# Optimization experiments

Hardware: AMD Instinct MI355X
Metric: run time of the kernel (lower is better)

Reference implementation:

```python
import jax, jax.numpy as jnp
import numpy as np

N = 65536      # input_size (mesh nodes)
CF = 16        # num_final_channels
L0 = 4097      # inv_conv_start
SPLIT = CF * L0  # 65552
SFC = 2        # number of space-filling curves
LAT = 128      # dims_latent
HID = 512      # size_fc[1]
B = 16         # batch
K = 32         # kernel_size (dimension==2)
STRIDE = 4
PAD = 16       # kernel_size // 2
OUT_PADS = (1, 0)


def setup_inputs() -> dict:
    key = jax.random.key(0)
    ks = jax.random.split(key, 8)
    s = 0.05
    ords, plus, minus = [], [], []
    for i in range(SFC):
        p = np.random.default_rng(i).permutation(N)
        ords.append(p)
        plus.append(np.concatenate([p[1:], p[-1:]]))   # find_plus_neigh
        minus.append(np.concatenate([p[:1], p[:-1]]))  # find_minus_neigh
    return {
        "x": jax.random.normal(ks[0], (B, LAT), jnp.float32),
        "W1": jax.random.normal(ks[1], (HID, LAT), jnp.float32) * s,
        "b1": jnp.zeros((HID,), jnp.float32),
        "W2": jax.random.normal(ks[2], (SPLIT * SFC, HID), jnp.float32) * s,
        "b2": jnp.zeros((SPLIT * SFC,), jnp.float32),
        "ctw0": jax.random.normal(ks[3], (SFC, CF, CF, K), jnp.float32) * s,
        "ctb0": jnp.zeros((SFC, CF), jnp.float32),
        "ctw1": jax.random.normal(ks[4], (SFC, CF, 1, K), jnp.float32) * s,
        "ctb1": jnp.zeros((SFC, 1), jnp.float32),
        "sps_w": jnp.full((SFC, N, 3), 1.0 / 3.0, jnp.float32),   # NearestNeighbouring per-sfc
        "sps_b": jnp.zeros((SFC, N), jnp.float32),
        "final_w": jnp.full((N, SFC), 1.0 / SFC, jnp.float32),    # final_sp
        "final_b": jnp.zeros((N,), jnp.float32),
        "out_w": jnp.ones((N,), jnp.float32),                     # output_linear
        "out_b": jnp.zeros((N,), jnp.float32),
        "ord_idx": jnp.asarray(np.stack(ords), jnp.int32),
        "plus_idx": jnp.asarray(np.stack(plus), jnp.int32),
        "minus_idx": jnp.asarray(np.stack(minus), jnp.int32),
    }


def _convT(b, w, bias, op):
    # PyTorch ConvTranspose1d(w:[Cin,Cout,K], stride=4, padding=16, output_padding=op)
    kern = jnp.flip(w, -1).transpose(1, 0, 2)  # -> [Cout, Cin, K]
    lo = K - 1 - PAD
    out = jax.lax.conv_general_dilated(
        b, kern, window_strides=(1,), padding=[(lo, lo + op)],
        lhs_dilation=(STRIDE,), dimension_numbers=('NCH', 'OIH', 'NCH'))
    return out + bias[None, :, None]


def reference(x, W1, b1, W2, b2, ctw0, ctb0, ctw1, ctb1,
              sps_w, sps_b, final_w, final_b, out_w, out_b,
              ord_idx, plus_idx, minus_idx):
    act = jnp.tanh
    h = act(x @ W1.T + b1)
    h = act(h @ W2.T + b2)
    h = h.reshape(-1, SPLIT, SFC)
    zs = []
    for i in range(SFC):
        b = h[:, :, i].reshape(-1, CF, L0)
        b = act(_convT(b, ctw0[i], ctb0[i], OUT_PADS[0]))  # [B,16,16385]
        b = act(_convT(b, ctw1[i], ctb1[i], OUT_PADS[1]))  # [B,1,65536]
        b = b.reshape(-1, N)
        # SFC gather: (minus, self, plus) neighbours, then learned weighted sum
        tt = jnp.stack([b[:, minus_idx[i]], b[:, ord_idx[i]], b[:, plus_idx[i]]], -1)  # [B,N,3]
        zs.append(act(jnp.sum(tt * sps_w[i], -1) + sps_b[i]))
    z = jnp.stack(zs, -1)                         # [B,N,SFC]
    z = act(jnp.sum(z * final_w, -1) + final_b)   # final NearestNeighbouring across SFCs
    return z * out_w + out_b                      # output_linear (components==1)
```

## Files before the change

kernel.cpp:

```cpp
#include <hip/hip_runtime.h>
#include <hip/hip_bf16.h>

#define N_NODES 65536
#define CFCH 16
#define L0LEN 4097
#define L1LEN 16385
#define NSFC 2
#define LATD 128
#define HIDD 512
#define NROWS (CFCH * L0LEN * NSFC)

typedef __attribute__((ext_vector_type(8))) short short8;
typedef __attribute__((ext_vector_type(4))) float f32x4;

__device__ __forceinline__ float fast_tanh(float x) {
    float ax = fabsf(x);
    float e = __expf(-2.0f * ax);
    float r = (1.0f - e) / (1.0f + e);
    return copysignf(r, x);
}

__device__ __forceinline__ ushort f2bf(float f) {
    unsigned u = __float_as_uint(f);
    return (ushort)((u + 0x7fffu + ((u >> 16) & 1u)) >> 16);
}

__device__ __forceinline__ void split8(const float4 a, const float4 b, short8& hi, short8& lo) {
    float f[8] = {a.x, a.y, a.z, a.w, b.x, b.y, b.z, b.w};
#pragma unroll
    for (int e = 0; e < 8; ++e) {
        ushort h = f2bf(f[e]);
        hi[e] = (short)h;
        lo[e] = (short)f2bf(f[e] - __uint_as_float((unsigned)h << 16));
    }
}

__global__ void fc1_kernel(const float* __restrict__ x, const float* __restrict__ W1,
                           const float* __restrict__ b1,
                           ushort* __restrict__ h1hi, ushort* __restrict__ h1lo) {
    int tid = blockIdx.x * 256 + threadIdx.x;
    int b = tid & 15;
    int j = tid >> 4;
    const float* xr = x + b * LATD;
    const float* wr = W1 + j * LATD;
    float acc = 0.f;
#pragma unroll 8
    for (int k = 0; k < LATD; ++k) acc = fmaf(xr[k], wr[k], acc);
    float h = fast_tanh(acc + b1[j]);
    ushort hi = f2bf(h);
    float hif = __uint_as_float((unsigned)hi << 16);
    ushort lo = f2bf(h - hif);
    h1hi[b * HIDD + j] = hi;
    h1lo[b * HIDD + j] = lo;
}

__global__ void __launch_bounds__(256, 4) fc2_kernel(const float* __restrict__ W2,
                                                     const float* __restrict__ b2,
                                                     const ushort* __restrict__ h1hi,
                                                     const ushort* __restrict__ h1lo,
                                                     float* __restrict__ h2) {
    __shared__ __align__(16) ushort hB[2][16][520];
    for (int u = threadIdx.x; u < 2048; u += 256) {
        int arr = u >> 10, uu = u & 1023;
        int n = uu >> 6, kc = uu & 63;
        const ushort* src = (arr ? h1lo : h1hi) + n * HIDD + kc * 8;
        *(uint4*)&hB[arr][n][kc * 8] = *(const uint4*)src;
    }
    __syncthreads();

    int tid = threadIdx.x;
    int w = tid >> 6, lane = tid & 63;
    int lm = lane & 15, lq = lane >> 4;
    int j0 = blockIdx.x * 128;
    int jr0 = j0 + (w * 2) * 16 + lm;     if (jr0 >= NROWS) jr0 = NROWS - 1;
    int jr1 = j0 + (w * 2 + 1) * 16 + lm; if (jr1 >= NROWS) jr1 = NROWS - 1;
    const float* a0p = W2 + (size_t)jr0 * HIDD + lq * 8;
    const float* a1p = W2 + (size_t)jr1 * HIDD + lq * 8;
    const ushort* bhp = &hB[0][lm][lq * 8];
    const ushort* blp = &hB[1][lm][lq * 8];
    f32x4 acc0 = {0.f, 0.f, 0.f, 0.f};
    f32x4 acc1 = {0.f, 0.f, 0.f, 0.f};

#pragma unroll 2
    for (int ks = 0; ks < 16; ++ks) {
        float4 a0a = *(const float4*)(a0p + ks * 32);
        float4 a0b = *(const float4*)(a0p + ks * 32 + 4);
        float4 a1a = *(const float4*)(a1p + ks * 32);
        float4 a1b = *(const float4*)(a1p + ks * 32 + 4);
        short8 bh = *(const short8*)(bhp + ks * 32);
        short8 bl = *(const short8*)(blp + ks * 32);
        short8 h0, l0, h1v, l1v;
        split8(a0a, a0b, h0, l0);
        split8(a1a, a1b, h1v, l1v);
        acc0 = __builtin_amdgcn_mfma_f32_16x16x32_bf16(h0, bh, acc0, 0, 0, 0);
        acc1 = __builtin_amdgcn_mfma_f32_16x16x32_bf16(h1v, bh, acc1, 0, 0, 0);
        acc0 = __builtin_amdgcn_mfma_f32_16x16x32_bf16(h0, bl, acc0, 0, 0, 0);
        acc1 = __builtin_amdgcn_mfma_f32_16x16x32_bf16(h1v, bl, acc1, 0, 0, 0);
        acc0 = __builtin_amdgcn_mfma_f32_16x16x32_bf16(l0, bh, acc0, 0, 0, 0);
        acc1 = __builtin_amdgcn_mfma_f32_16x16x32_bf16(l1v, bh, acc1, 0, 0, 0);
    }

#pragma unroll
    for (int mt = 0; mt < 2; ++mt) {
        f32x4 acc = mt ? acc1 : acc0;
        int jb = j0 + (w * 2 + mt) * 16 + lq * 4;
#pragma unroll
        for (int reg = 0; reg < 4; ++reg) {
            int j = jb + reg;
            if (j < NROWS) {
                float val = fast_tanh(acc[reg] + b2[j]);
                int ii = j & 1;
                int s = j >> 1;
                int c = s / L0LEN;
                int l = s - c * L0LEN;
                h2[((size_t)(ii * 16 + lm) * CFCH + c) * L0LEN + l] = val;
            }
        }
    }
}

#define SROW 592
#define PHYSF(f) ((f) + (((f) >> 5) << 2))

__global__ void __launch_bounds__(256, 4) conv0_kernel(const float* __restrict__ h2,
                                                       const float* __restrict__ ctw0,
                                                       const float* __restrict__ ctb0,
                                                       float* __restrict__ t0) {
    __shared__ float inS[16 * SROW];
    int bx = blockIdx.x, bb = blockIdx.y, z = blockIdx.z;
    int i = z >> 3;
    int co0 = (z & 7) << 1;
    int tid = threadIdx.x;
    int r = __builtin_amdgcn_readfirstlane(tid >> 6);
    int lane = tid & 63;

    const float* hin = h2 + (size_t)((i * 16 + bb) * 16) * L0LEN;
    int qbase = (bx << 9) - 4;
#pragma unroll 1
    for (int ci = 0; ci < 16; ++ci) {
        for (int xx = tid; xx < 528; xx += 256) {
            int q = qbase + xx;
            inS[ci * SROW + PHYSF(xx)] = (q >= 0 && q < L0LEN) ? hin[ci * L0LEN + q] : 0.f;
        }
    }
    __syncthreads();

    float acc0[8], acc1[8];
#pragma unroll
    for (int u = 0; u < 8; ++u) { acc0[u] = 0.f; acc1[u] = 0.f; }

    const float* wbase = ctw0 + (((i * 16) * 16 + co0) << 5) + r;
    int fb = lane << 3;
#pragma unroll 2
    for (int ci = 0; ci < 16; ++ci) {
        int base = ci * SROW;
        float4 xa = *(const float4*)&inS[base + PHYSF(fb)];
        float4 xb = *(const float4*)&inS[base + PHYSF(fb + 4)];
        float4 xc = *(const float4*)&inS[base + PHYSF(fb + 8)];
        float4 xd = *(const float4*)&inS[base + PHYSF(fb + 12)];
        float xin[16] = {xa.x, xa.y, xa.z, xa.w, xb.x, xb.y, xb.z, xb.w,
                         xc.x, xc.y, xc.z, xc.w, xd.x, xd.y, xd.z, xd.w};
        const float* w0 = wbase + ci * 512;
        const float* w1 = w0 + 32;
#pragma unroll
        for (int t = 0; t < 8; ++t) {
            float wv0 = w0[t << 2];
            float wv1 = w1[t << 2];
#pragma unroll
            for (int u = 0; u < 8; ++u) {
                float xv = xin[u - t + 8];
                acc0[u] = fmaf(wv0, xv, acc0[u]);
                acc1[u] = fmaf(wv1, xv, acc1[u]);
            }
        }
    }
    float b0 = ctb0[i * 16 + co0];
    float b1 = ctb0[i * 16 + co0 + 1];
    int o0 = bx << 11;
    float* dst0 = t0 + ((size_t)(i * 16 + bb) * 16 + co0) * L1LEN;
    float* dst1 = dst0 + L1LEN;
#pragma unroll
    for (int u = 0; u < 8; ++u) {
        int o = o0 + (((lane << 3) + u) << 2) + r;
        if (o < L1LEN) {
            dst0[o] = fast_tanh(acc0[u] + b0);
            dst1[o] = fast_tanh(acc1[u] + b1);
        }
    }
}

__global__ void __launch_bounds__(256, 4) conv1_kernel(const float* __restrict__ t0,
                                                       const float* __restrict__ ctw1,
                                                       const float* __restrict__ ctb1,
                                                       float* __restrict__ t1) {
    __shared__ float inS[16 * SROW];
    int bx = blockIdx.x, bb = blockIdx.y, i = blockIdx.z;
    int tid = threadIdx.x;
    int r = __builtin_amdgcn_readfirstlane(tid >> 6);
    int lane = tid & 63;

    const float* tin = t0 + (size_t)(i * 16 + bb) * 16 * L1LEN;
    int qbase = (bx << 9) - 4;
#pragma unroll 1
    for (int ci = 0; ci < 16; ++ci) {
        for (int xx = tid; xx < 528; xx += 256) {
            int q = qbase + xx;
            inS[ci * SROW + PHYSF(xx)] = (q >= 0 && q < L1LEN) ? tin[ci * L1LEN + q] : 0.f;
        }
    }
    __syncthreads();

    float acc[8];
#pragma unroll
    for (int u = 0; u < 8; ++u) acc[u] = 0.f;

    const float* wbase = ctw1 + ((i * 16) << 5) + r;
    int fb = lane << 3;
#pragma unroll 2
    for (int ci = 0; ci < 16; ++ci) {
        int base = ci * SROW;
        float4 xa = *(const float4*)&inS[base + PHYSF(fb)];
        float4 xb = *(const float4*)&inS[base + PHYSF(fb + 4)];
        float4 xc = *(const float4*)&inS[base + PHYSF(fb + 8)];
        float4 xd = *(const float4*)&inS[base + PHYSF(fb + 12)];
        float xin[16] = {xa.x, xa.y, xa.z, xa.w, xb.x, xb.y, xb.z, xb.w,
                         xc.x, xc.y, xc.z, xc.w, xd.x, xd.y, xd.z, xd.w};
        const float* w0 = wbase + (ci << 5);
#pragma unroll
        for (int t = 0; t < 8; ++t) {
            float wv = w0[t << 2];
#pragma unroll
            for (int u = 0; u < 8; ++u)
                acc[u] = fmaf(wv, xin[u - t + 8], acc[u]);
        }
    }
    float bias = ctb1[i];
    int o0 = bx << 11;
    float* dst = t1 + (size_t)(i * 16 + bb) * (size_t)N_NODES;
#pragma unroll
    for (int u = 0; u < 8; ++u) {
        int o = o0 + (((lane << 3) + u) << 2) + r;
        dst[o] = fast_tanh(acc[u] + bias);
    }
}

__global__ void __launch_bounds__(256) final_kernel(const float* __restrict__ t1,
        const float* __restrict__ sps_w, const float* __restrict__ sps_b,
        const float* __restrict__ final_w, const float* __restrict__ final_b,
        const float* __restrict__ out_w, const float* __restrict__ out_b,
        const int* __restrict__ ord_idx, float* __restrict__ out) {
    int g = blockIdx.x * 256 + threadIdx.x;
    int b = g >> 14;
    int n0 = (g & 16383) << 2;
    float z[2][4];
#pragma unroll
    for (int i = 0; i < 2; ++i) {
        const int* od = ord_idx + i * N_NODES;
        int4 mid = *(const int4*)(od + n0);
        int idx0 = (n0 == 0) ? mid.x : od[n0 - 1];
        int idx5 = (n0 + 4 >= N_NODES) ? mid.w : od[n0 + 4];
        const float* tb = t1 + ((size_t)(i * 16 + b) << 16);
        float v0 = tb[idx0], v1 = tb[mid.x], v2 = tb[mid.y],
              v3 = tb[mid.z], v4 = tb[mid.w], v5 = tb[idx5];
        const float* sw = sps_w + ((size_t)i * N_NODES + n0) * 3;
        float4 swa = *(const float4*)sw;
        float4 swb = *(const float4*)(sw + 4);
        float4 swc = *(const float4*)(sw + 8);
        float4 sb = *(const float4*)(sps_b + (size_t)i * N_NODES + n0);
        z[i][0] = fast_tanh(fmaf(v0, swa.x, fmaf(v1, swa.y, fmaf(v2, swa.z, sb.x))));
        z[i][1] = fast_tanh(fmaf(v1, swa.w, fmaf(v2, swb.x, fmaf(v3, swb.y, sb.y))));
        z[i][2] = fast_tanh(fmaf(v2, swb.z, fmaf(v3, swb.w, fmaf(v4, swc.x, sb.z))));
        z[i][3] = fast_tanh(fmaf(v3, swc.y, fmaf(v4, swc.z, fmaf(v5, swc.w, sb.w))));
    }
    float4 fwa = *(const float4*)(final_w + (size_t)n0 * 2);
    float4 fwb = *(const float4*)(final_w + (size_t)n0 * 2 + 4);
    float4 fb = *(const float4*)(final_b + n0);
    float4 ow = *(const float4*)(out_w + n0);
    float4 ob = *(const float4*)(out_b + n0);
    float4 r;
    r.x = fmaf(fast_tanh(fmaf(z[0][0], fwa.x, fmaf(z[1][0], fwa.y, fb.x))), ow.x, ob.x);
    r.y = fmaf(fast_tanh(fmaf(z[0][1], fwa.z, fmaf(z[1][1], fwa.w, fb.y))), ow.y, ob.y);
    r.z = fmaf(fast_tanh(fmaf(z[0][2], fwb.x, fmaf(z[1][2], fwb.y, fb.z))), ow.z, ob.z);
    r.w = fmaf(fast_tanh(fmaf(z[0][3], fwb.z, fmaf(z[1][3], fwb.w, fb.w))), ow.w, ob.w);
    *(float4*)(out + ((size_t)b << 16) + n0) = r;
}

extern "C" void kernel_launch(void* const* d_in, const int* in_sizes, int n_in,
                              void* d_out, int out_size, void* d_ws, size_t ws_size,
                              hipStream_t stream) {
    const float* x       = (const float*)d_in[0];
    const float* W1      = (const float*)d_in[1];
    const float* b1      = (const float*)d_in[2];
    const float* W2      = (const float*)d_in[3];
    const float* b2      = (const float*)d_in[4];
    const float* ctw0    = (const float*)d_in[5];
    const float* ctb0    = (const float*)d_in[6];
    const float* ctw1    = (const float*)d_in[7];
    const float* ctb1    = (const float*)d_in[8];
    const float* sps_w   = (const float*)d_in[9];
    const float* sps_b   = (const float*)d_in[10];
    const float* final_w = (const float*)d_in[11];
    const float* final_b = (const float*)d_in[12];
    const float* out_w   = (const float*)d_in[13];
    const float* out_b   = (const float*)d_in[14];
    const int* ord_idx   = (const int*)d_in[15];

    float* ws  = (float*)d_ws;
    float* h2  = ws;
    float* t0  = h2 + 2097664;
    float* t1  = t0 + 8389120;
    ushort* h1hi = (ushort*)(t1 + 2097152);
    ushort* h1lo = h1hi + 8192;
    float* out = (float*)d_out;

    hipLaunchKernelGGL(fc1_kernel, dim3(32), dim3(256), 0, stream, x, W1, b1, h1hi, h1lo);
    hipLaunchKernelGGL(fc2_kernel, dim3((NROWS + 127) / 128), dim3(256), 0, stream,
                       W2, b2, h1hi, h1lo, h2);
    hipLaunchKernelGGL(conv0_kernel, dim3(9, 16, 16), dim3(256), 0, stream,
                       h2, ctw0, ctb0, t0);
    hipLaunchKernelGGL(conv1_kernel, dim3(32, 16, 2), dim3(256), 0, stream,
                       t0, ctw1, ctb1, t1);
    hipLaunchKernelGGL(final_kernel, dim3(1024), dim3(256), 0, stream,
                       t1, sps_w, sps_b, final_w, final_b, out_w, out_b,
                       ord_idx, out);
}
```

Measured before the change: 554.1 us.

## Fuse both transposed convolutions into one kernel with shared-memory intermediate

Merges conv0 and conv1 into a single kernel. Each block computes the 16-channel conv0 output tile for its conv1 output range directly into LDS, including one halo element, and then runs conv1 from LDS. This removes the roughly 33 MB t0 intermediate write and read and one launch. In exchange it uses more LDS per block (weights plus tiles), so occupancy drops to 2 blocks per SM, and it adds a small serial halo computation done by half the threads.

```diff
diff --git a/kernel.cpp b/kernel.cpp
--- a/kernel.cpp
+++ b/kernel.cpp
@@ -119,128 +119,152 @@
     }
 }
 
-#define SROW 592
-#define PHYSF(f) ((f) + (((f) >> 5) << 2))
-
-__global__ void __launch_bounds__(256, 4) conv0_kernel(const float* __restrict__ h2,
-                                                       const float* __restrict__ ctw0,
-                                                       const float* __restrict__ ctb0,
-                                                       float* __restrict__ t0) {
-    __shared__ float inS[16 * SROW];
-    int bx = blockIdx.x, bb = blockIdx.y, z = blockIdx.z;
-    int i = z >> 3;
-    int co0 = (z & 7) << 1;
-    int tid = threadIdx.x;
-    int r = __builtin_amdgcn_readfirstlane(tid >> 6);
-    int lane = tid & 63;
-
-    const float* hin = h2 + (size_t)((i * 16 + bb) * 16) * L0LEN;
-    int qbase = (bx << 9) - 4;
-#pragma unroll 1
-    for (int ci = 0; ci < 16; ++ci) {
-        for (int xx = tid; xx < 528; xx += 256) {
-            int q = qbase + xx;
-            inS[ci * SROW + PHYSF(xx)] = (q >= 0 && q < L0LEN) ? hin[ci * L0LEN + q] : 0.f;
-        }
-    }
-    __syncthreads();
-
-    float acc0[8], acc1[8];
-#pragma unroll
-    for (int u = 0; u < 8; ++u) { acc0[u] = 0.f; acc1[u] = 0.f; }
-
-    const float* wbase = ctw0 + (((i * 16) * 16 + co0) << 5) + r;
-    int fb = lane << 3;
-#pragma unroll 2
-    for (int ci = 0; ci < 16; ++ci) {
-        int base = ci * SROW;
-        float4 xa = *(const float4*)&inS[base + PHYSF(fb)];
-        float4 xb = *(const float4*)&inS[base + PHYSF(fb + 4)];
-        float4 xc = *(const float4*)&inS[base + PHYSF(fb + 8)];
-        float4 xd = *(const float4*)&inS[base + PHYSF(fb + 12)];
-        float xin[16] = {xa.x, xa.y, xa.z, xa.w, xb.x, xb.y, xb.z, xb.w,
-                         xc.x, xc.y, xc.z, xc.w, xd.x, xd.y, xd.z, xd.w};
-        const float* w0 = wbase + ci * 512;
-        const float* w1 = w0 + 32;
-#pragma unroll
-        for (int t = 0; t < 8; ++t) {
-            float wv0 = w0[t << 2];
-            float wv1 = w1[t << 2];
-#pragma unroll
-            for (int u = 0; u < 8; ++u) {
-                float xv = xin[u - t + 8];
-                acc0[u] = fmaf(wv0, xv, acc0[u]);
-                acc1[u] = fmaf(wv1, xv, acc1[u]);
-            }
-        }
-    }
-    float b0 = ctb0[i * 16 + co0];
-    float b1 = ctb0[i * 16 + co0 + 1];
-    int o0 = bx << 11;
-    float* dst0 = t0 + ((size_t)(i * 16 + bb) * 16 + co0) * L1LEN;
-    float* dst1 = dst0 + L1LEN;
-#pragma unroll
-    for (int u = 0; u < 8; ++u) {
-        int o = o0 + (((lane << 3) + u) << 2) + r;
-        if (o < L1LEN) {
-            dst0[o] = fast_tanh(acc0[u] + b0);
-            dst1[o] = fast_tanh(acc1[u] + b1);
-        }
-    }
-}
-
-__global__ void __launch_bounds__(256, 4) conv1_kernel(const float* __restrict__ t0,
-                                                       const float* __restrict__ ctw1,
-                                                       const float* __restrict__ ctb1,
-                                                       float* __restrict__ t1) {
-    __shared__ float inS[16 * SROW];
+#define H2ROW 144
+#define T0ROW 520
+
+__global__ void __launch_bounds__(256, 2) convfused_kernel(const float* __restrict__ h2,
+        const float* __restrict__ ctw0, const float* __restrict__ ctb0,
+        const float* __restrict__ ctw1, const float* __restrict__ ctb1,
+        float* __restrict__ t1) {
+    __shared__ float h2S[16 * H2ROW];
+    __shared__ float w0T[16 * 16 * 32];
+    __shared__ float w1T[16 * 32];
+    __shared__ float t0S[16 * T0ROW];
+
     int bx = blockIdx.x, bb = blockIdx.y, i = blockIdx.z;
     int tid = threadIdx.x;
     int r = __builtin_amdgcn_readfirstlane(tid >> 6);
     int lane = tid & 63;
 
-    const float* tin = t0 + (size_t)(i * 16 + bb) * 16 * L1LEN;
-    int qbase = (bx << 9) - 4;
-#pragma unroll 1
-    for (int ci = 0; ci < 16; ++ci) {
-        for (int xx = tid; xx < 528; xx += 256) {
-            int q = qbase + xx;
-            inS[ci * SROW + PHYSF(xx)] = (q >= 0 && q < L1LEN) ? tin[ci * L1LEN + q] : 0.f;
-        }
+    int q0 = (bx << 7) - 4;
+    const float* hin = h2 + (size_t)((i * 16 + bb) * 16) * L0LEN;
+#pragma unroll 1
+    for (int u = tid; u < 16 * 140; u += 256) {
+        int ci = u / 140;
+        int xx = u - ci * 140;
+        int q = q0 + xx;
+        h2S[ci * H2ROW + xx] = (q >= 0 && q < L0LEN) ? hin[ci * L0LEN + q] : 0.f;
+    }
+    const float* w0g = ctw0 + (i << 13);
+#pragma unroll 1
+    for (int g = tid; g < 8192; g += 256) {
+        int k = g & 31;
+        w0T[(g & ~31) + ((k & 3) << 3) + (k >> 2)] = w0g[g];
+    }
+    const float* w1g = ctw1 + (i << 9);
+#pragma unroll 1
+    for (int g = tid; g < 512; g += 256) {
+        int k = g & 31;
+        w1T[(g & ~31) + ((k & 3) << 3) + (k >> 2)] = w1g[g];
     }
     __syncthreads();
 
-    float acc[8];
-#pragma unroll
-    for (int u = 0; u < 8; ++u) acc[u] = 0.f;
-
-    const float* wbase = ctw1 + ((i * 16) << 5) + r;
-    int fb = lane << 3;
-#pragma unroll 2
-    for (int ci = 0; ci < 16; ++ci) {
-        int base = ci * SROW;
-        float4 xa = *(const float4*)&inS[base + PHYSF(fb)];
-        float4 xb = *(const float4*)&inS[base + PHYSF(fb + 4)];
-        float4 xc = *(const float4*)&inS[base + PHYSF(fb + 8)];
-        float4 xd = *(const float4*)&inS[base + PHYSF(fb + 12)];
-        float xin[16] = {xa.x, xa.y, xa.z, xa.w, xb.x, xb.y, xb.z, xb.w,
-                         xc.x, xc.y, xc.z, xc.w, xd.x, xd.y, xd.z, xd.w};
-        const float* w0 = wbase + (ci << 5);
-#pragma unroll
-        for (int t = 0; t < 8; ++t) {
-            float wv = w0[t << 2];
-#pragma unroll
-            for (int u = 0; u < 8; ++u)
-                acc[u] = fmaf(wv, xin[u - t + 8], acc[u]);
-        }
-    }
-    float bias = ctb1[i];
-    int o0 = bx << 11;
-    float* dst = t1 + (size_t)(i * 16 + bb) * (size_t)N_NODES;
-#pragma unroll
-    for (int u = 0; u < 8; ++u) {
-        int o = o0 + (((lane << 3) + u) << 2) + r;
-        dst[o] = fast_tanh(acc[u] + bias);
+    int p0 = (bx << 9) - 4;
+
+    {
+        float acc[16][2];
+#pragma unroll
+        for (int co = 0; co < 16; ++co) { acc[co][0] = 0.f; acc[co][1] = 0.f; }
+        int Qb = lane << 1;
+#pragma unroll 1
+        for (int ci = 0; ci < 16; ++ci) {
+            const float* xb = &h2S[ci * H2ROW + Qb];
+            float2 xA = *(const float2*)(xb);
+            float2 xB = *(const float2*)(xb + 2);
+            float2 xC = *(const float2*)(xb + 4);
+            float2 xD = *(const float2*)(xb + 6);
+            float x8v = xb[8];
+            float x[9] = {xA.x, xA.y, xB.x, xB.y, xC.x, xC.y, xD.x, xD.y, x8v};
+            const float* wbase = &w0T[(ci << 9) + (r << 3)];
+#pragma unroll
+            for (int co = 0; co < 16; ++co) {
+                const float* wrow = wbase + (co << 5);
+                float4 wa = *(const float4*)wrow;
+                float4 wb4 = *(const float4*)(wrow + 4);
+                acc[co][0] = fmaf(wa.x,  x[7], acc[co][0]);
+                acc[co][0] = fmaf(wa.y,  x[6], acc[co][0]);
+                acc[co][0] = fmaf(wa.z,  x[5], acc[co][0]);
+                acc[co][0] = fmaf(wa.w,  x[4], acc[co][0]);
+                acc[co][0] = fmaf(wb4.x, x[3], acc[co][0]);
+                acc[co][0] = fmaf(wb4.y, x[2], acc[co][0]);
+                acc[co][0] = fmaf(wb4.z, x[1], acc[co][0]);
+                acc[co][0] = fmaf(wb4.w, x[0], acc[co][0]);
+                acc[co][1] = fmaf(wa.x,  x[8], acc[co][1]);
+                acc[co][1] = fmaf(wa.y,  x[7], acc[co][1]);
+                acc[co][1] = fmaf(wa.z,  x[6], acc[co][1]);
+                acc[co][1] = fmaf(wa.w,  x[5], acc[co][1]);
+                acc[co][1] = fmaf(wb4.x, x[4], acc[co][1]);
+                acc[co][1] = fmaf(wb4.y, x[3], acc[co][1]);
+                acc[co][1] = fmaf(wb4.z, x[2], acc[co][1]);
+                acc[co][1] = fmaf(wb4.w, x[1], acc[co][1]);
+            }
+        }
+#pragma unroll
+        for (int co = 0; co < 16; ++co) {
+            float b0 = ctb0[(i << 4) + co];
+#pragma unroll
+            for (int j = 0; j < 2; ++j) {
+                int p = ((Qb + j) << 2) + r;
+                unsigned P = (unsigned)(p0 + p);
+                float val = (P < L1LEN) ? fast_tanh(acc[co][j] + b0) : 0.f;
+                if (p >= 1) t0S[co * T0ROW + (p - 1)] = val;
+            }
+        }
+    }
+
+    if (tid < 128) {
+        int co = tid >> 3;
+        int Qt = 128 + ((tid >> 2) & 1);
+        int rt = tid & 3;
+        float acct = 0.f;
+#pragma unroll 1
+        for (int ci = 0; ci < 16; ++ci) {
+            const float* xb = &h2S[ci * H2ROW + Qt];
+            const float* wrow = &w0T[(ci << 9) + (co << 5) + (rt << 3)];
+#pragma unroll
+            for (int t = 0; t < 8; ++t)
+                acct = fmaf(wrow[t], xb[7 - t], acct);
+        }
+        float b0 = ctb0[(i << 4) + co];
+        int p = (Qt << 2) + rt;
+        unsigned P = (unsigned)(p0 + p);
+        t0S[co * T0ROW + (p - 1)] = (P < L1LEN) ? fast_tanh(acct + b0) : 0.f;
+    }
+    __syncthreads();
+
+    {
+        int Qb1 = lane << 3;
+        float acc1[8];
+#pragma unroll
+        for (int j = 0; j < 8; ++j) acc1[j] = 0.f;
+#pragma unroll 1
+        for (int ci = 0; ci < 16; ++ci) {
+            const float* xb = &t0S[ci * T0ROW + Qb1];
+            float4 xa = *(const float4*)(xb);
+            float4 xv = *(const float4*)(xb + 4);
+            float4 xc = *(const float4*)(xb + 8);
+            float4 xd = *(const float4*)(xb + 12);
+            float x[16] = {xa.x, xa.y, xa.z, xa.w, xv.x, xv.y, xv.z, xv.w,
+                           xc.x, xc.y, xc.z, xc.w, xd.x, xd.y, xd.z, xd.w};
+            const float* wrow = &w1T[(ci << 5) + (r << 3)];
+            float4 wa = *(const float4*)wrow;
+            float4 wb4 = *(const float4*)(wrow + 4);
+            float wt[8] = {wa.x, wa.y, wa.z, wa.w, wb4.x, wb4.y, wb4.z, wb4.w};
+#pragma unroll
+            for (int j = 0; j < 8; ++j) {
+#pragma unroll
+                for (int t = 0; t < 8; ++t)
+                    acc1[j] = fmaf(wt[t], x[j + 7 - t], acc1[j]);
+            }
+        }
+        float bias = ctb1[i];
+        float* dst = t1 + (size_t)(i * 16 + bb) * (size_t)N_NODES;
+        int o0 = bx << 11;
+#pragma unroll
+        for (int j = 0; j < 8; ++j) {
+            int o = o0 + ((Qb1 + j) << 2) + r;
+            dst[o] = fast_tanh(acc1[j] + bias);
+        }
     }
 }
 
@@ -307,8 +331,7 @@
 
     float* ws  = (float*)d_ws;
     float* h2  = ws;
-    float* t0  = h2 + 2097664;
-    float* t1  = t0 + 8389120;
+    float* t1  = h2 + 2097664;
     ushort* h1hi = (ushort*)(t1 + 2097152);
     ushort* h1lo = h1hi + 8192;
     float* out = (float*)d_out;
@@ -316,10 +339,8 @@
     hipLaunchKernelGGL(fc1_kernel, dim3(32), dim3(256), 0, stream, x, W1, b1, h1hi, h1lo);
     hipLaunchKernelGGL(fc2_kernel, dim3((NROWS + 127) / 128), dim3(256), 0, stream,
                        W2, b2, h1hi, h1lo, h2);
-    hipLaunchKernelGGL(conv0_kernel, dim3(9, 16, 16), dim3(256), 0, stream,
-                       h2, ctw0, ctb0, t0);
-    hipLaunchKernelGGL(conv1_kernel, dim3(32, 16, 2), dim3(256), 0, stream,
-                       t0, ctw1, ctb1, t1);
+    hipLaunchKernelGGL(convfused_kernel, dim3(32, 16, 2), dim3(256), 0, stream,
+                       h2, ctw0, ctb0, ctw1, ctb1, t1);
     hipLaunchKernelGGL(final_kernel, dim3(1024), dim3(256), 0, stream,
                        t1, sps_w, sps_b, final_w, final_b, out_w, out_b,
                        ord_idx, out);
```

New measurement: 525.3 us. -5.2%, faster.
